# Performance work log

Measured on AMD Instinct MI355X. Metric: run time of the kernel, lower is better.

The kernel has to match this reference:

```python
import jax, jax.numpy as jnp
import numpy as np

B, C, D, K = 65536, 128, 32, 10
EPS = 1e-12


def setup_inputs() -> dict:
    key = jax.random.key(0)
    k1, k2, k3, k4 = jax.random.split(key, 4)
    data = jax.random.normal(k1, (B, D), dtype=jnp.float32)
    mu = jax.random.normal(k2, (C, D), dtype=jnp.float32)
    # S_inv must be symmetric positive definite (inverse covariance per cluster)
    A = 0.1 * jax.random.normal(k3, (C, D, D), dtype=jnp.float32)
    S_inv = jnp.einsum('cij,ckj->cik', A, A) + jnp.eye(D, dtype=jnp.float32)[None]
    # one-hot class assignment per cluster (int32), as stored in the module
    cls = jax.random.randint(k4, (C,), 0, K)
    cluster_labels = jax.nn.one_hot(cls, K, dtype=jnp.int32)
    return {"data": data, "mu": mu, "S_inv": S_inv, "cluster_labels": cluster_labels}


def reference(data, mu, S_inv, cluster_labels):
    # Mahalanobis distance d2[b,c] = (z_b - mu_c)^T S_inv_c (z_b - mu_c),
    # expanded to avoid a [B, C, D] diff tensor.
    zz = data[:, :, None] * data[:, None, :]            # [B, D, D]
    t1 = jnp.einsum('bde,cde->bc', zz, S_inv)           # z' Sinv z
    Sm = jnp.einsum('cde,ce->cd', S_inv, mu)            # [C, D]
    t2 = data @ Sm.T                                    # z' Sinv mu  [B, C]
    t3 = jnp.einsum('cd,cd->c', mu, Sm)                 # mu' Sinv mu [C]
    d2 = t1 - 2.0 * t2 + t3[None, :]                    # [B, C]
    Gamma = jnp.exp(-0.5 * d2)                          # Gaussian activation
    # defuzzify_batch: normalize activations, project through one-hot labels
    norm_gamma = Gamma / (jnp.sum(Gamma, axis=1, keepdims=True) + EPS)
    label_scores = norm_gamma @ cluster_labels.astype(jnp.float32)  # [B, K]
    preds = jnp.argmax(label_scores, axis=1)
    clusters = jnp.argmax(Gamma, axis=1)
    return label_scores, preds, clusters
```

## Files before the change

kernel.cpp:

```cpp
#include <hip/hip_runtime.h>
#include <cmath>

#define B_N 65536
#define C_N 128
#define D_N 32
#define K_N 10
#define EPS_F 1e-12f
#define SCALE_F (-0.72134752044448169f)

#define NKK 46
#define CHUNK_F16 4096
#define QF_N (NKK * CHUNK_F16)
#define YSTR 41

typedef _Float16 f16x8 __attribute__((ext_vector_type(8)));
typedef float    f32x16 __attribute__((ext_vector_type(16)));

__device__ __forceinline__ void mdkk(int kk, int& dA, int& e0) {
    if (kk >= 45) { dA = 0; e0 = 0; return; }
    int w = (kk >= 17) + (kk >= 30) + (kk >= 39) + (kk >= 44);
    int off = w == 0 ? 0 : (w == 1 ? 17 : (w == 2 ? 30 : (w == 3 ? 39 : 44)));
    int r = kk - off;
    dA = 2 * r;
    e0 = 2 * r + 8 * w;
}

__global__ __launch_bounds__(128) void k_prep(const float* __restrict__ S,
                                              const float* __restrict__ mu,
                                              const int* __restrict__ onehot,
                                              _Float16* __restrict__ QF,
                                              int* __restrict__ cls) {
    const int c = blockIdx.x;
    const int tid = threadIdx.x;
    __shared__ float sSm[D_N];
    __shared__ float st3;

    if (tid < D_N) {
        const float* Sr = S + (size_t)c * (D_N * D_N) + (size_t)tid * D_N;
        const float* mr = mu + (size_t)c * D_N;
        float a0 = 0.f, a1 = 0.f;
#pragma unroll
        for (int e = 0; e < D_N; e += 2) {
            a0 = fmaf(Sr[e + 0], mr[e + 0], a0);
            a1 = fmaf(Sr[e + 1], mr[e + 1], a1);
        }
        sSm[tid] = a0 + a1;
    }
    __syncthreads();
    if (tid == 0) {
        const float* mr = mu + (size_t)c * D_N;
        float a = 0.f;
#pragma unroll
        for (int d = 0; d < D_N; ++d) a = fmaf(mr[d], sSm[d], a);
        st3 = a;
        int cl = 0;
#pragma unroll
        for (int k = 0; k < K_N; ++k)
            if (onehot[c * K_N + k] != 0) cl = k;
        cls[c] = cl;
    }
    __syncthreads();

    if (tid < 2 * NKK) {
        const int kk   = tid >> 1;
        const int half = tid & 1;
        int dA, e0;
        mdkk(kk, dA, e0);
        const int d  = dA + half;
        const int ct = c >> 5;
        const size_t base = (size_t)kk * CHUNK_F16 + ct * 1024
                          + (size_t)(half * 32 + (c & 31)) * 8;
        const float* Sc = S + (size_t)c * (D_N * D_N);
        for (int j = 0; j < 8; ++j) {
            const int e = e0 + j;
            float q = 0.f;
            if (kk < 45 && d <= e && e <= 32) {
                float v;
                if (e < 32)      v = Sc[d * D_N + e] * (d == e ? 1.f : 2.f);
                else if (d < 32) v = -2.f * sSm[d];
                else             v = st3;
                q = SCALE_F * v;
            }
            _Float16 h = (_Float16)q;
            QF[base + j]       = h;
            QF[base + 512 + j] = (_Float16)(q - (float)h);
        }
    }
}

__device__ __forceinline__ void gl_lds16(const void* g, void* l) {
    __builtin_amdgcn_global_load_lds(
        (const __attribute__((address_space(1))) unsigned int*)g,
        (__attribute__((address_space(3))) unsigned int*)l, 16, 0, 0);
}

__device__ __forceinline__ void stage_chunk(const _Float16* __restrict__ QF,
                                            _Float16* __restrict__ dst,
                                            int chunk, int wid, int lane) {
#pragma unroll
    for (int i = 0; i < 2; ++i) {
        const int slot = i * 4 + wid;
        gl_lds16(QF + (size_t)chunk * CHUNK_F16 + slot * 512 + lane * 8,
                 dst + slot * 512);
    }
}

__device__ __forceinline__ void ldy(const float* sy, int ybase, int hioff,
                                    int kk, float& yd, float (&yw)[8]) {
    int dA, e0;
    mdkk(kk, dA, e0);
    yd = sy[ybase + dA + hioff];
#pragma unroll
    for (int j = 0; j < 8; ++j) yw[j] = sy[ybase + e0 + j];
}

__device__ __forceinline__ void step_compute(const _Float16* __restrict__ buf,
                                             int lane, float yd, const float (&yw)[8],
                                             f32x16 (&acc)[4]) {
    const f16x8* qb = (const f16x8*)buf;
    f16x8 qh[4], ql[4];
#pragma unroll
    for (int ct = 0; ct < 4; ++ct) {
        qh[ct] = qb[ct * 128 + lane];
        ql[ct] = qb[ct * 128 + 64 + lane];
    }
    f16x8 ph, pl;
#pragma unroll
    for (int j = 0; j < 8; j += 2) {
        float f0 = yd * yw[j], f1 = yd * yw[j + 1];
        auto h2 = __builtin_amdgcn_cvt_pkrtz(f0, f1);
        float r0 = f0 - (float)h2[0];
        float r1 = f1 - (float)h2[1];
        auto l2 = __builtin_amdgcn_cvt_pkrtz(r0, r1);
        ph[j] = h2[0]; ph[j + 1] = h2[1];
        pl[j] = l2[0]; pl[j + 1] = l2[1];
    }
#pragma unroll
    for (int ct = 0; ct < 4; ++ct)
        acc[ct] = __builtin_amdgcn_mfma_f32_32x32x16_f16(qh[ct], ph, acc[ct], 0, 0, 0);
#pragma unroll
    for (int ct = 0; ct < 4; ++ct)
        acc[ct] = __builtin_amdgcn_mfma_f32_32x32x16_f16(ql[ct], ph, acc[ct], 0, 0, 0);
#pragma unroll
    for (int ct = 0; ct < 4; ++ct)
        acc[ct] = __builtin_amdgcn_mfma_f32_32x32x16_f16(qh[ct], pl, acc[ct], 0, 0, 0);
}

__global__ __launch_bounds__(256, 2) void k_mainv6(const float* __restrict__ data,
                                                   const _Float16* __restrict__ QF,
                                                   const int* __restrict__ clsp,
                                                   float* __restrict__ out) {
    const int tid  = threadIdx.x;
    const int lane = tid & 63;
    const int wid  = tid >> 6;
    const int b0w  = blockIdx.x * 128 + wid * 32;
    const int col  = lane & 31;
    const bool hi  = lane >= 32;

    __shared__ float sy[256 * YSTR + 64];
    __shared__ alignas(16) _Float16 qbuf[2][CHUNK_F16];
    __shared__ int lcls[C_N];
    if (tid < C_N) lcls[tid] = clsp[tid];

    const int ybase = tid * YSTR;
    {
        const float4* p0 = (const float4*)(data + (size_t)(b0w + col) * D_N);
#pragma unroll
        for (int i = 0; i < 8; ++i) {
            float4 v = p0[i];
            sy[ybase + 4 * i + 0] = v.x;
            sy[ybase + 4 * i + 1] = v.y;
            sy[ybase + 4 * i + 2] = v.z;
            sy[ybase + 4 * i + 3] = v.w;
        }
        sy[ybase + 32] = 1.f;
#pragma unroll
        for (int i = 33; i < YSTR; ++i) sy[ybase + i] = 0.f;
        if (tid < 64) sy[256 * YSTR + tid] = 0.f;
    }

    f32x16 acc[4];
#pragma unroll
    for (int ct = 0; ct < 4; ++ct)
#pragma unroll
        for (int g = 0; g < 16; ++g) acc[ct][g] = 0.f;

    stage_chunk(QF, &qbuf[0][0], 0, wid, lane);
    stage_chunk(QF, &qbuf[1][0], 1, wid, lane);
    __syncthreads();

    const int hioff = hi ? 1 : 0;
    float ydA, ywA[8], ydB, ywB[8];
    ldy(sy, ybase, hioff, 0, ydA, ywA);

#pragma clang loop unroll(disable)
    for (int t = 0; t < NKK; t += 2) {
        ldy(sy, ybase, hioff, t + 1, ydB, ywB);
        step_compute(&qbuf[0][0], lane, ydA, ywA, acc);
        __syncthreads();
        if (t + 2 < NKK) stage_chunk(QF, &qbuf[0][0], t + 2, wid, lane);
        ldy(sy, ybase, hioff, t + 2, ydA, ywA);
        step_compute(&qbuf[1][0], lane, ydB, ywB, acc);
        __syncthreads();
        if (t + 3 < NKK) stage_chunk(QF, &qbuf[1][0], t + 3, wid, lane);
    }

    const float hoff = hi ? 4.f : 0.f;
    const int* lc = lcls + (hi ? 4 : 0);
    float sum = 0.f, gmax = -1.f, gcf = 0.f;
    float a0 = 0, a1 = 0, a2 = 0, a3 = 0, a4 = 0, a5 = 0, a6 = 0, a7 = 0, a8 = 0, a9 = 0;
#pragma unroll
    for (int ct = 0; ct < 4; ++ct) {
        float psum = 0.f;
#pragma unroll
        for (int g = 0; g < 16; ++g) {
            float v = acc[ct][g];
            float gm;
            asm("v_exp_f32 %0, %1" : "=v"(gm) : "v"(v));
            const int cbase = ct * 32 + (g & 3) + 8 * (g >> 2);
            int cl = lc[cbase];
            psum += gm;
            float cf = (float)cbase + hoff;
            if (gm > gmax) { gmax = gm; gcf = cf; }
            a0 += (cl == 0) ? gm : 0.f;
            a1 += (cl == 1) ? gm : 0.f;
            a2 += (cl == 2) ? gm : 0.f;
            a3 += (cl == 3) ? gm : 0.f;
            a4 += (cl == 4) ? gm : 0.f;
            a5 += (cl == 5) ? gm : 0.f;
            a6 += (cl == 6) ? gm : 0.f;
            a7 += (cl == 7) ? gm : 0.f;
            a8 += (cl == 8) ? gm : 0.f;
            a9 += (cl == 9) ? gm : 0.f;
        }
        sum += psum;
    }

    sum += __shfl_xor(sum, 32, 64);
    {
        float om = __shfl_xor(gmax, 32, 64);
        float oc = __shfl_xor(gcf, 32, 64);
        bool take = (om > gmax) || (om == gmax && oc < gcf);
        if (take) { gmax = om; gcf = oc; }
    }
    a0 += __shfl_xor(a0, 32, 64);
    a1 += __shfl_xor(a1, 32, 64);
    a2 += __shfl_xor(a2, 32, 64);
    a3 += __shfl_xor(a3, 32, 64);
    a4 += __shfl_xor(a4, 32, 64);
    a5 += __shfl_xor(a5, 32, 64);
    a6 += __shfl_xor(a6, 32, 64);
    a7 += __shfl_xor(a7, 32, 64);
    a8 += __shfl_xor(a8, 32, 64);
    a9 += __shfl_xor(a9, 32, 64);

    if (!hi) {
        const int b = b0w + col;
        float inv = 1.0f / (sum + EPS_F);
        float ls[K_N] = {a0 * inv, a1 * inv, a2 * inv, a3 * inv, a4 * inv,
                         a5 * inv, a6 * inv, a7 * inv, a8 * inv, a9 * inv};
        float best = -1.f;
        int bk = 0;
#pragma unroll
        for (int k = 0; k < K_N; ++k)
            if (ls[k] > best) { best = ls[k]; bk = k; }
        float2* o2 = (float2*)(out + (size_t)b * K_N);
#pragma unroll
        for (int k2 = 0; k2 < K_N / 2; ++k2)
            o2[k2] = make_float2(ls[2 * k2], ls[2 * k2 + 1]);
        out[(size_t)B_N * K_N + b] = (float)bk;
        out[(size_t)B_N * K_N + B_N + b] = gcf;
    }
}

extern "C" void kernel_launch(void* const* d_in, const int* in_sizes, int n_in,
                              void* d_out, int out_size, void* d_ws, size_t ws_size,
                              hipStream_t stream) {
    const float* data   = (const float*)d_in[0];
    const float* mu     = (const float*)d_in[1];
    const float* S      = (const float*)d_in[2];
    const int*   onehot = (const int*)d_in[3];
    float* out = (float*)d_out;

    _Float16* QF  = (_Float16*)d_ws;
    int*      cls = (int*)(QF + QF_N);

    hipLaunchKernelGGL(k_prep, dim3(C_N), dim3(128), 0, stream,
                       S, mu, onehot, QF, cls);
    hipLaunchKernelGGL(k_mainv6, dim3(B_N / 128), dim3(256), 0, stream,
                       data, QF, cls, out);
}
```

Before: 106.6 us.

## Split K-loop across wave pairs and load Q fragments directly from global

Blocks grow to 512 threads. Each pair of waves shares one 32-row group and splits the 45 live k-chunks in half, then reduces the partial accumulators through an LDS scratch buffer before the epilogue. The LDS double-buffered staging of QF and its per-step barriers are dropped: each wave now reads the Q fragments straight from global (L2-resident) memory, with the next phi prefetched. This aims for more latency hiding and fewer barriers, at the cost of redundant global loads per wave, a cross-wave reduction, and an epilogue where half the waves sit idle.

After: 114.7 us. 7.5% more time.

```diff
diff --git a/kernel.cpp b/kernel.cpp
--- a/kernel.cpp
+++ b/kernel.cpp
@@ -8,10 +8,12 @@
 #define EPS_F 1e-12f
 #define SCALE_F (-0.72134752044448169f)
 
-#define NKK 46
+#define NKK 48
+#define NLIVE 45
 #define CHUNK_F16 4096
 #define QF_N (NKK * CHUNK_F16)
-#define YSTR 41
+#define YSTR 33
+#define SMEM_BYTES 67584
 
 typedef _Float16 f16x8 __attribute__((ext_vector_type(8)));
 typedef float    f32x16 __attribute__((ext_vector_type(16)));
@@ -88,96 +90,88 @@
     }
 }
 
-__device__ __forceinline__ void gl_lds16(const void* g, void* l) {
-    __builtin_amdgcn_global_load_lds(
-        (const __attribute__((address_space(1))) unsigned int*)g,
-        (__attribute__((address_space(3))) unsigned int*)l, 16, 0, 0);
-}
-
-__device__ __forceinline__ void stage_chunk(const _Float16* __restrict__ QF,
-                                            _Float16* __restrict__ dst,
-                                            int chunk, int wid, int lane) {
-#pragma unroll
-    for (int i = 0; i < 2; ++i) {
-        const int slot = i * 4 + wid;
-        gl_lds16(QF + (size_t)chunk * CHUNK_F16 + slot * 512 + lane * 8,
-                 dst + slot * 512);
-    }
-}
-
-__device__ __forceinline__ void ldy(const float* sy, int ybase, int hioff,
-                                    int kk, float& yd, float (&yw)[8]) {
+__device__ __forceinline__ void mkphi_at(const float* __restrict__ yrow,
+                                         int hioff, int t,
+                                         f16x8& ph, f16x8& pl) {
     int dA, e0;
-    mdkk(kk, dA, e0);
-    yd = sy[ybase + dA + hioff];
-#pragma unroll
-    for (int j = 0; j < 8; ++j) yw[j] = sy[ybase + e0 + j];
-}
-
-__device__ __forceinline__ void step_compute(const _Float16* __restrict__ buf,
-                                             int lane, float yd, const float (&yw)[8],
-                                             f32x16 (&acc)[4]) {
-    const f16x8* qb = (const f16x8*)buf;
-    f16x8 qh[4], ql[4];
-#pragma unroll
-    for (int ct = 0; ct < 4; ++ct) {
-        qh[ct] = qb[ct * 128 + lane];
-        ql[ct] = qb[ct * 128 + 64 + lane];
-    }
-    f16x8 ph, pl;
-#pragma unroll
-    for (int j = 0; j < 8; j += 2) {
-        float f0 = yd * yw[j], f1 = yd * yw[j + 1];
+    mdkk(t, dA, e0);
+    const float yd = yrow[dA + hioff];
+    union { unsigned int w[4]; f16x8 v; } H, L;
+#pragma unroll
+    for (int p = 0; p < 4; ++p) {
+        float f0 = yd * yrow[e0 + 2 * p];
+        float f1 = yd * yrow[e0 + 2 * p + 1];
         auto h2 = __builtin_amdgcn_cvt_pkrtz(f0, f1);
         float r0 = f0 - (float)h2[0];
         float r1 = f1 - (float)h2[1];
         auto l2 = __builtin_amdgcn_cvt_pkrtz(r0, r1);
-        ph[j] = h2[0]; ph[j + 1] = h2[1];
-        pl[j] = l2[0]; pl[j + 1] = l2[1];
-    }
+        __builtin_memcpy(&H.w[p], &h2, 4);
+        __builtin_memcpy(&L.w[p], &l2, 4);
+    }
+    ph = H.v;
+    pl = L.v;
+}
+
+__device__ __forceinline__ void scr_write(float* __restrict__ base, int lane,
+                                          const f32x16 (&acc)[4]) {
 #pragma unroll
     for (int ct = 0; ct < 4; ++ct)
-        acc[ct] = __builtin_amdgcn_mfma_f32_32x32x16_f16(qh[ct], ph, acc[ct], 0, 0, 0);
+#pragma unroll
+        for (int gq = 0; gq < 4; ++gq) {
+            const int g4 = ct * 4 + gq;
+            const int fo = lane * 132 + (((g4 + 2 * lane) & 31) << 2);
+            *(float4*)(base + fo) = make_float4(acc[ct][4 * gq + 0], acc[ct][4 * gq + 1],
+                                                acc[ct][4 * gq + 2], acc[ct][4 * gq + 3]);
+        }
+}
+__device__ __forceinline__ void scr_read_add(const float* __restrict__ base, int lane,
+                                             f32x16 (&acc)[4]) {
 #pragma unroll
     for (int ct = 0; ct < 4; ++ct)
-        acc[ct] = __builtin_amdgcn_mfma_f32_32x32x16_f16(ql[ct], ph, acc[ct], 0, 0, 0);
-#pragma unroll
-    for (int ct = 0; ct < 4; ++ct)
-        acc[ct] = __builtin_amdgcn_mfma_f32_32x32x16_f16(qh[ct], pl, acc[ct], 0, 0, 0);
-}
-
-__global__ __launch_bounds__(256, 2) void k_mainv6(const float* __restrict__ data,
-                                                   const _Float16* __restrict__ QF,
-                                                   const int* __restrict__ clsp,
-                                                   float* __restrict__ out) {
+#pragma unroll
+        for (int gq = 0; gq < 4; ++gq) {
+            const int g4 = ct * 4 + gq;
+            const int fo = lane * 132 + (((g4 + 2 * lane) & 31) << 2);
+            float4 v = *(const float4*)(base + fo);
+            acc[ct][4 * gq + 0] += v.x; acc[ct][4 * gq + 1] += v.y;
+            acc[ct][4 * gq + 2] += v.z; acc[ct][4 * gq + 3] += v.w;
+        }
+}
+
+__global__ __launch_bounds__(512, 4) void k_mainv12(const float* __restrict__ data,
+                                                    const _Float16* __restrict__ QF,
+                                                    const int* __restrict__ clsp,
+                                                    float* __restrict__ out) {
     const int tid  = threadIdx.x;
     const int lane = tid & 63;
     const int wid  = tid >> 6;
-    const int b0w  = blockIdx.x * 128 + wid * 32;
+    const int rg   = wid >> 1;
+    const int kh   = wid & 1;
     const int col  = lane & 31;
     const bool hi  = lane >= 32;
-
-    __shared__ float sy[256 * YSTR + 64];
-    __shared__ alignas(16) _Float16 qbuf[2][CHUNK_F16];
+    const int bb   = blockIdx.x * 128;
+
+    __shared__ __attribute__((aligned(16))) char smem[SMEM_BYTES];
     __shared__ int lcls[C_N];
+    float* sy = (float*)smem;
+
     if (tid < C_N) lcls[tid] = clsp[tid];
-
-    const int ybase = tid * YSTR;
-    {
-        const float4* p0 = (const float4*)(data + (size_t)(b0w + col) * D_N);
+    if (tid < 128) {
+        const float4* p0 = (const float4*)(data + (size_t)(bb + tid) * D_N);
+        const int yb = tid * YSTR;
 #pragma unroll
         for (int i = 0; i < 8; ++i) {
             float4 v = p0[i];
-            sy[ybase + 4 * i + 0] = v.x;
-            sy[ybase + 4 * i + 1] = v.y;
-            sy[ybase + 4 * i + 2] = v.z;
-            sy[ybase + 4 * i + 3] = v.w;
-        }
-        sy[ybase + 32] = 1.f;
-#pragma unroll
-        for (int i = 33; i < YSTR; ++i) sy[ybase + i] = 0.f;
-        if (tid < 64) sy[256 * YSTR + tid] = 0.f;
-    }
+            sy[yb + 4 * i + 0] = v.x;
+            sy[yb + 4 * i + 1] = v.y;
+            sy[yb + 4 * i + 2] = v.z;
+            sy[yb + 4 * i + 3] = v.w;
+        }
+        sy[yb + 32] = 1.f;
+    } else if (tid < 192) {
+        sy[128 * YSTR + (tid - 128)] = 0.f;
+    }
+    __syncthreads();
 
     f32x16 acc[4];
 #pragma unroll
@@ -185,91 +179,117 @@
 #pragma unroll
         for (int g = 0; g < 16; ++g) acc[ct][g] = 0.f;
 
-    stage_chunk(QF, &qbuf[0][0], 0, wid, lane);
-    stage_chunk(QF, &qbuf[1][0], 1, wid, lane);
-    __syncthreads();
-
+    const f16x8* qg = (const f16x8*)QF;
+    const float* yrow = sy + (rg * 32 + col) * YSTR;
     const int hioff = hi ? 1 : 0;
-    float ydA, ywA[8], ydB, ywB[8];
-    ldy(sy, ybase, hioff, 0, ydA, ywA);
+    const int start = kh * 23;
+    const int end   = kh ? NLIVE : 23;
+
+    f16x8 phc, plc;
+    mkphi_at(yrow, hioff, start, phc, plc);
 
 #pragma clang loop unroll(disable)
-    for (int t = 0; t < NKK; t += 2) {
-        ldy(sy, ybase, hioff, t + 1, ydB, ywB);
-        step_compute(&qbuf[0][0], lane, ydA, ywA, acc);
-        __syncthreads();
-        if (t + 2 < NKK) stage_chunk(QF, &qbuf[0][0], t + 2, wid, lane);
-        ldy(sy, ybase, hioff, t + 2, ydA, ywA);
-        step_compute(&qbuf[1][0], lane, ydB, ywB, acc);
-        __syncthreads();
-        if (t + 3 < NKK) stage_chunk(QF, &qbuf[1][0], t + 3, wid, lane);
-    }
-
-    const float hoff = hi ? 4.f : 0.f;
-    const int* lc = lcls + (hi ? 4 : 0);
-    float sum = 0.f, gmax = -1.f, gcf = 0.f;
-    float a0 = 0, a1 = 0, a2 = 0, a3 = 0, a4 = 0, a5 = 0, a6 = 0, a7 = 0, a8 = 0, a9 = 0;
-#pragma unroll
-    for (int ct = 0; ct < 4; ++ct) {
-        float psum = 0.f;
-#pragma unroll
-        for (int g = 0; g < 16; ++g) {
-            float v = acc[ct][g];
-            float gm;
-            asm("v_exp_f32 %0, %1" : "=v"(gm) : "v"(v));
-            const int cbase = ct * 32 + (g & 3) + 8 * (g >> 2);
-            int cl = lc[cbase];
-            psum += gm;
-            float cf = (float)cbase + hoff;
-            if (gm > gmax) { gmax = gm; gcf = cf; }
-            a0 += (cl == 0) ? gm : 0.f;
-            a1 += (cl == 1) ? gm : 0.f;
-            a2 += (cl == 2) ? gm : 0.f;
-            a3 += (cl == 3) ? gm : 0.f;
-            a4 += (cl == 4) ? gm : 0.f;
-            a5 += (cl == 5) ? gm : 0.f;
-            a6 += (cl == 6) ? gm : 0.f;
-            a7 += (cl == 7) ? gm : 0.f;
-            a8 += (cl == 8) ? gm : 0.f;
-            a9 += (cl == 9) ? gm : 0.f;
-        }
-        sum += psum;
-    }
-
-    sum += __shfl_xor(sum, 32, 64);
-    {
-        float om = __shfl_xor(gmax, 32, 64);
-        float oc = __shfl_xor(gcf, 32, 64);
-        bool take = (om > gmax) || (om == gmax && oc < gcf);
-        if (take) { gmax = om; gcf = oc; }
-    }
-    a0 += __shfl_xor(a0, 32, 64);
-    a1 += __shfl_xor(a1, 32, 64);
-    a2 += __shfl_xor(a2, 32, 64);
-    a3 += __shfl_xor(a3, 32, 64);
-    a4 += __shfl_xor(a4, 32, 64);
-    a5 += __shfl_xor(a5, 32, 64);
-    a6 += __shfl_xor(a6, 32, 64);
-    a7 += __shfl_xor(a7, 32, 64);
-    a8 += __shfl_xor(a8, 32, 64);
-    a9 += __shfl_xor(a9, 32, 64);
-
-    if (!hi) {
-        const int b = b0w + col;
-        float inv = 1.0f / (sum + EPS_F);
-        float ls[K_N] = {a0 * inv, a1 * inv, a2 * inv, a3 * inv, a4 * inv,
-                         a5 * inv, a6 * inv, a7 * inv, a8 * inv, a9 * inv};
-        float best = -1.f;
-        int bk = 0;
-#pragma unroll
-        for (int k = 0; k < K_N; ++k)
-            if (ls[k] > best) { best = ls[k]; bk = k; }
-        float2* o2 = (float2*)(out + (size_t)b * K_N);
-#pragma unroll
-        for (int k2 = 0; k2 < K_N / 2; ++k2)
-            o2[k2] = make_float2(ls[2 * k2], ls[2 * k2 + 1]);
-        out[(size_t)B_N * K_N + b] = (float)bk;
-        out[(size_t)B_N * K_N + B_N + b] = gcf;
+    for (int t = start; t < end; ++t) {
+        const f16x8* p = qg + (size_t)t * 512 + lane;
+        f16x8 qh0 = p[0],   ql0 = p[64];
+        f16x8 qh1 = p[128], ql1 = p[192];
+        f16x8 qh2 = p[256], ql2 = p[320];
+        f16x8 qh3 = p[384], ql3 = p[448];
+        f16x8 phn, pln;
+        mkphi_at(yrow, hioff, t + 1, phn, pln);
+        acc[0] = __builtin_amdgcn_mfma_f32_32x32x16_f16(qh0, phc, acc[0], 0, 0, 0);
+        acc[1] = __builtin_amdgcn_mfma_f32_32x32x16_f16(qh1, phc, acc[1], 0, 0, 0);
+        acc[2] = __builtin_amdgcn_mfma_f32_32x32x16_f16(qh2, phc, acc[2], 0, 0, 0);
+        acc[3] = __builtin_amdgcn_mfma_f32_32x32x16_f16(qh3, phc, acc[3], 0, 0, 0);
+        acc[0] = __builtin_amdgcn_mfma_f32_32x32x16_f16(ql0, phc, acc[0], 0, 0, 0);
+        acc[1] = __builtin_amdgcn_mfma_f32_32x32x16_f16(ql1, phc, acc[1], 0, 0, 0);
+        acc[2] = __builtin_amdgcn_mfma_f32_32x32x16_f16(ql2, phc, acc[2], 0, 0, 0);
+        acc[3] = __builtin_amdgcn_mfma_f32_32x32x16_f16(ql3, phc, acc[3], 0, 0, 0);
+        acc[0] = __builtin_amdgcn_mfma_f32_32x32x16_f16(qh0, plc, acc[0], 0, 0, 0);
+        acc[1] = __builtin_amdgcn_mfma_f32_32x32x16_f16(qh1, plc, acc[1], 0, 0, 0);
+        acc[2] = __builtin_amdgcn_mfma_f32_32x32x16_f16(qh2, plc, acc[2], 0, 0, 0);
+        acc[3] = __builtin_amdgcn_mfma_f32_32x32x16_f16(qh3, plc, acc[3], 0, 0, 0);
+        phc = phn;
+        plc = pln;
+    }
+
+    float* scrf = (float*)smem;
+    __syncthreads();
+    if (rg < 2 && kh == 1) scr_write(scrf + (rg & 1) * 8448, lane, acc);
+    __syncthreads();
+    if (rg < 2 && kh == 0) scr_read_add(scrf + (rg & 1) * 8448, lane, acc);
+    __syncthreads();
+    if (rg >= 2 && kh == 1) scr_write(scrf + (rg & 1) * 8448, lane, acc);
+    __syncthreads();
+    if (rg >= 2 && kh == 0) scr_read_add(scrf + (rg & 1) * 8448, lane, acc);
+
+    if (kh == 0) {
+        const float hoff = hi ? 4.f : 0.f;
+        const int* lc = lcls + (hi ? 4 : 0);
+        float sum = 0.f, gmax = -1.f, gcf = 0.f;
+        float a0 = 0, a1 = 0, a2 = 0, a3 = 0, a4 = 0, a5 = 0, a6 = 0, a7 = 0, a8 = 0, a9 = 0;
+#pragma unroll
+        for (int ct = 0; ct < 4; ++ct) {
+            float psum = 0.f;
+#pragma unroll
+            for (int g = 0; g < 16; ++g) {
+                float v = acc[ct][g];
+                float gm;
+                asm("v_exp_f32 %0, %1" : "=v"(gm) : "v"(v));
+                const int cbase = ct * 32 + (g & 3) + 8 * (g >> 2);
+                int cl = lc[cbase];
+                psum += gm;
+                float cf = (float)cbase + hoff;
+                if (gm > gmax) { gmax = gm; gcf = cf; }
+                a0 += (cl == 0) ? gm : 0.f;
+                a1 += (cl == 1) ? gm : 0.f;
+                a2 += (cl == 2) ? gm : 0.f;
+                a3 += (cl == 3) ? gm : 0.f;
+                a4 += (cl == 4) ? gm : 0.f;
+                a5 += (cl == 5) ? gm : 0.f;
+                a6 += (cl == 6) ? gm : 0.f;
+                a7 += (cl == 7) ? gm : 0.f;
+                a8 += (cl == 8) ? gm : 0.f;
+                a9 += (cl == 9) ? gm : 0.f;
+            }
+            sum += psum;
+        }
+
+        sum += __shfl_xor(sum, 32, 64);
+        {
+            float om = __shfl_xor(gmax, 32, 64);
+            float oc = __shfl_xor(gcf, 32, 64);
+            bool take = (om > gmax) || (om == gmax && oc < gcf);
+            if (take) { gmax = om; gcf = oc; }
+        }
+        a0 += __shfl_xor(a0, 32, 64);
+        a1 += __shfl_xor(a1, 32, 64);
+        a2 += __shfl_xor(a2, 32, 64);
+        a3 += __shfl_xor(a3, 32, 64);
+        a4 += __shfl_xor(a4, 32, 64);
+        a5 += __shfl_xor(a5, 32, 64);
+        a6 += __shfl_xor(a6, 32, 64);
+        a7 += __shfl_xor(a7, 32, 64);
+        a8 += __shfl_xor(a8, 32, 64);
+        a9 += __shfl_xor(a9, 32, 64);
+
+        if (!hi) {
+            const int b = bb + rg * 32 + col;
+            float inv = 1.0f / (sum + EPS_F);
+            float ls[K_N] = {a0 * inv, a1 * inv, a2 * inv, a3 * inv, a4 * inv,
+                             a5 * inv, a6 * inv, a7 * inv, a8 * inv, a9 * inv};
+            float best = -1.f;
+            int bk = 0;
+#pragma unroll
+            for (int k = 0; k < K_N; ++k)
+                if (ls[k] > best) { best = ls[k]; bk = k; }
+            float2* o2 = (float2*)(out + (size_t)b * K_N);
+#pragma unroll
+            for (int k2 = 0; k2 < K_N / 2; ++k2)
+                o2[k2] = make_float2(ls[2 * k2], ls[2 * k2 + 1]);
+            out[(size_t)B_N * K_N + b] = (float)bk;
+            out[(size_t)B_N * K_N + B_N + b] = gcf;
+        }
     }
 }
 
@@ -287,6 +307,6 @@
 
     hipLaunchKernelGGL(k_prep, dim3(C_N), dim3(128), 0, stream,
                        S, mu, onehot, QF, cls);
-    hipLaunchKernelGGL(k_mainv6, dim3(B_N / 128), dim3(256), 0, stream,
+    hipLaunchKernelGGL(k_mainv12, dim3(B_N / 128), dim3(512), 0, stream,
                        data, QF, cls, out);
 }
```
